# Kernel optimization log

Measured on AMD Instinct MI355X. Metric: run time of the kernel, lower is better.

The kernel has to match this reference:

```python
import jax, jax.numpy as jnp
import numpy as np

HEADS = 8

def _rotate_every_two(t):
    # t: [..., d]; interleaved rotation (-x2, x1) pairs
    x1 = t[..., ::2]
    x2 = t[..., 1::2]
    return jnp.stack([-x2, x1], axis=-1).reshape(t.shape)

def _theta_shift(t, sin, cos):
    return t * cos + _rotate_every_two(t) * sin

def setup_inputs() -> dict:
    key = jax.random.key(0)
    ks = jax.random.split(key, 5)
    B, H, W, C = 4, 40, 40, 512
    dh = C // HEADS
    x = jax.random.normal(ks[0], (B, H, W, C), dtype=jnp.float32)
    sin = jax.random.normal(ks[1], (H, W, dh), dtype=jnp.float32)
    cos = jax.random.normal(ks[2], (H, W, dh), dtype=jnp.float32)
    # 1x1 conv weight [3C, C] (kernel dims squeezed) + bias
    w_qkv = jax.random.normal(ks[3], (3 * C, C), dtype=jnp.float32) * (C ** -0.5)
    b_qkv = jnp.zeros((3 * C,), dtype=jnp.float32)
    return {"x": x, "sin": sin, "cos": cos, "w_qkv": w_qkv, "b_qkv": b_qkv}

def reference(x, sin, cos, w_qkv, b_qkv):
    B, H, W, C = x.shape
    heads = HEADS
    dh = C // heads
    scale = dh ** -0.5
    # 1x1 conv == per-pixel linear projection
    qkv = jnp.einsum('bhwc,oc->bhwo', x, w_qkv) + b_qkv  # [B,H,W,3C]
    q, k, v = jnp.split(qkv, 3, axis=-1)

    def to_heads(t):
        # channel order is (heads, dim_head) per the torch rearrange
        return t.reshape(B, H, W, heads, dh).transpose(0, 3, 1, 2, 4)  # [B,heads,H,W,dh]

    q = _theta_shift(to_heads(q), sin, cos)
    k = _theta_shift(to_heads(k), sin, cos)
    # v is computed but unused downstream in the original module (bug preserved)

    N = H * W
    q = q.reshape(B, heads, N, dh)
    k = k.reshape(B, heads, N, dh)

    attn = jnp.einsum('bhnd,bhmd->bhnm', q, k) * scale  # [B,heads,N,N]
    p = jax.nn.softmax(attn, axis=-1)
    # NOTE: original code does matmul(logist, kfine_heads) — K, not V. Kept faithful.
    out = jnp.einsum('bhnm,bhmd->bhnd', p, k)  # [B,heads,N,dh]
    out = out.transpose(0, 2, 1, 3).reshape(B, H, W, C)
    return out
```

## Files before the change

### kernel.cpp

```cpp
#include <hip/hip_runtime.h>
#include <hip/hip_bf16.h>


typedef __hip_bfloat16 bf16;
typedef __attribute__((ext_vector_type(8))) short short8;
typedef __attribute__((ext_vector_type(4))) short bfx4;
typedef __attribute__((ext_vector_type(4))) float f32x4;

#define NSP 1600
#define CDIM 512
#define DH 64

__device__ __forceinline__ f32x4 mfma32(short8 a, short8 b, f32x4 c) {
  return __builtin_amdgcn_mfma_f32_16x16x32_bf16(a, b, c, 0, 0, 0);
}

#if __has_builtin(__builtin_amdgcn_mfma_f32_16x16x16bf16_1k)
__device__ __forceinline__ f32x4 mfma_k16(bfx4 a, bfx4 b, f32x4 c) {
  return __builtin_amdgcn_mfma_f32_16x16x16bf16_1k(a, b, c, 0, 0, 0);
}
#else
__device__ __forceinline__ f32x4 mfma_k16(bfx4 a, bfx4 b, f32x4 c) {
  short8 a8 = {a.x, a.y, a.z, a.w, 0, 0, 0, 0};
  short8 b8 = {b.x, b.y, b.z, b.w, 0, 0, 0, 0};
  return __builtin_amdgcn_mfma_f32_16x16x32_bf16(a8, b8, c, 0, 0, 0);
}
#endif

__device__ __forceinline__ short8 cvt8(float4 v0, float4 v1) {
  short8 r; bf16* p = (bf16*)&r;
  p[0] = __float2bfloat16(v0.x); p[1] = __float2bfloat16(v0.y);
  p[2] = __float2bfloat16(v0.z); p[3] = __float2bfloat16(v0.w);
  p[4] = __float2bfloat16(v1.x); p[5] = __float2bfloat16(v1.y);
  p[6] = __float2bfloat16(v1.z); p[7] = __float2bfloat16(v1.w);
  return r;
}

extern "C" __global__ __launch_bounds__(256)
void cvt_kernel(const float* __restrict__ x, const float* __restrict__ w,
                const float* __restrict__ sin_t, const float* __restrict__ cos_t,
                bf16* __restrict__ x_bf, bf16* __restrict__ w_bf,
                float* __restrict__ sinT, float* __restrict__ cosT)
{
  __shared__ float t_lds[64][68];
  const int bid = blockIdx.x, tid = threadIdx.x;
  if (bid < 1600) {
    const size_t i = (size_t)bid * 2048 + tid * 8;
    float4 v0 = *(const float4*)(x + i);
    float4 v1 = *(const float4*)(x + i + 4);
    *(short8*)(x_bf + i) = cvt8(v0, v1);
  } else if (bid < 1856) {
    const size_t i = (size_t)(bid - 1600) * 2048 + tid * 8;
    float4 v0 = *(const float4*)(w + i);
    float4 v1 = *(const float4*)(w + i + 4);
    *(short8*)(w_bf + i) = cvt8(v0, v1);
  } else {
    const int t = bid - 1856;
    const float* src = (t < 25) ? sin_t : cos_t;
    float* dst = (t < 25) ? sinT : cosT;
    const int nt = (t < 25) ? t : t - 25;
    const int r = tid >> 2, c = (tid & 3) * 16;
#pragma unroll
    for (int j = 0; j < 4; ++j)
      *(float4*)&t_lds[r][c + j * 4] =
          *(const float4*)(src + (size_t)(nt * 64 + r) * 64 + c + j * 4);
    __syncthreads();
#pragma unroll
    for (int j4 = 0; j4 < 4; ++j4) {
      float4 o;
      o.x = t_lds[c + j4 * 4 + 0][r];
      o.y = t_lds[c + j4 * 4 + 1][r];
      o.z = t_lds[c + j4 * 4 + 2][r];
      o.w = t_lds[c + j4 * 4 + 3][r];
      *(float4*)(dst + (size_t)r * NSP + nt * 64 + c + j4 * 4) = o;
    }
  }
}

extern "C" __global__ __launch_bounds__(256)
void proj_kernel(const bf16* __restrict__ x_bf, const bf16* __restrict__ w_bf,
                 const float* __restrict__ bias, const float* __restrict__ sinT,
                 const float* __restrict__ cosT, bf16* __restrict__ q_ws,
                 bf16* __restrict__ k2_ws, bf16* __restrict__ kt2_ws)
{
  __shared__ __align__(16) char smem[36864];
  bf16 (*x_lds)[72] = (bf16(*)[72])smem;
  bf16 (*w_lds)[72] = (bf16(*)[72])(smem + 18432);
  bf16* ep = (bf16*)smem;

  const int tid  = threadIdx.x;
  const int wave = tid >> 6;
  const int lane = tid & 63;
  const int col  = lane & 15;
  const int quad = lane >> 4;
  const int wm = wave >> 1, wo = wave & 1;
  const int m0 = blockIdx.x * 128;
  const int o0 = blockIdx.y * 128;

  f32x4 acc[4][4];
#pragma unroll
  for (int i = 0; i < 4; ++i)
#pragma unroll
    for (int j = 0; j < 4; ++j) acc[i][j] = {0.f, 0.f, 0.f, 0.f};

  const int srow = tid >> 1;
  const int sch  = (tid & 1) * 32;

  for (int kt = 0; kt < 8; ++kt) {
    __syncthreads();
    {
      const bf16* xs = x_bf + (size_t)(m0 + srow) * CDIM + kt * 64 + sch;
      const bf16* ws = w_bf + (size_t)(o0 + srow) * CDIM + kt * 64 + sch;
#pragma unroll
      for (int j = 0; j < 4; ++j) {
        *(short8*)&x_lds[srow][sch + j * 8] = *(const short8*)(xs + j * 8);
        *(short8*)&w_lds[srow][sch + j * 8] = *(const short8*)(ws + j * 8);
      }
    }
    __syncthreads();
#pragma unroll
    for (int half = 0; half < 2; ++half) {
      short8 af[4], bfr[4];
#pragma unroll
      for (int mt = 0; mt < 4; ++mt)
        af[mt] = *(short8*)&x_lds[wm * 64 + mt * 16 + col][half * 32 + quad * 8];
#pragma unroll
      for (int ot = 0; ot < 4; ++ot)
        bfr[ot] = *(short8*)&w_lds[wo * 64 + ot * 16 + col][half * 32 + quad * 8];
#pragma unroll
      for (int mt = 0; mt < 4; ++mt)
#pragma unroll
        for (int ot = 0; ot < 4; ++ot)
          acc[mt][ot] = mfma32(af[mt], bfr[ot], acc[mt][ot]);
    }
  }

  __syncthreads();
  const int b_idx = (m0 + wm * 64) / NSP;
  const int n0w   = m0 + wm * 64 - b_idx * NSP;
  const bool isq  = (o0 < 512);
#pragma unroll
  for (int ot = 0; ot < 4; ++ot) {
    const int o_local = wo * 64 + ot * 16 + col;
    const int o_g = o0 + o_local;
    const float bv = bias[o_g];
    const int d = o_g & 63;
#pragma unroll
    for (int mt = 0; mt < 4; ++mt) {
      const int nl = mt * 16 + quad * 4;
      float t[4], rot[4];
#pragma unroll
      for (int r = 0; r < 4; ++r) t[r] = acc[mt][ot][r] + bv;
#pragma unroll
      for (int r = 0; r < 4; ++r) {
        float tp = __shfl_xor(t[r], 1, 64);
        rot[r] = (lane & 1) ? tp : -tp;
      }
      const float4 c4 = *(const float4*)(cosT + (size_t)d * NSP + n0w + nl);
      const float4 s4 = *(const float4*)(sinT + (size_t)d * NSP + n0w + nl);
      float res[4];
      res[0] = t[0] * c4.x + rot[0] * s4.x;
      res[1] = t[1] * c4.y + rot[1] * s4.y;
      res[2] = t[2] * c4.z + rot[2] * s4.z;
      res[3] = t[3] * c4.w + rot[3] * s4.w;
      if (isq) {
#pragma unroll
        for (int r = 0; r < 4; ++r) res[r] *= 0.125f;
      }
      bfx4 pk; bf16* pp = (bf16*)&pk;
#pragma unroll
      for (int r = 0; r < 4; ++r) pp[r] = __float2bfloat16(res[r]);
      *(bfx4*)&ep[o_local * 132 + wm * 64 + nl] = pk;
    }
  }
  __syncthreads();

  if (isq) {
    const int m_l = tid >> 1, half = tid & 1;
    const int gm = m0 + m_l;
    const int bi = gm / NSP, n = gm - bi * NSP;
    const int h = (o0 >> 6) + half;
    bf16* base = q_ws + ((size_t)(bi * 8 + h) * NSP + n) * 64;
#pragma unroll
    for (int c = 0; c < 8; ++c) {
      short8 v; bf16* vp = (bf16*)&v;
#pragma unroll
      for (int j = 0; j < 8; ++j) vp[j] = ep[(half * 64 + c * 8 + j) * 132 + m_l];
      *(short8*)(base + c * 8) = v;
    }
  } else {
    const int h0 = (o0 - 512) >> 6;
#pragma unroll
    for (int it = 0; it < 8; ++it) {
      const int ci = it * 256 + tid;
      const int hh = ci >> 10, T = (ci >> 9) & 1, inner = ci & 511;
      const int ccol = inner & 15, cq = (inner >> 4) & 3;
      const int f = (inner >> 6) & 1, ti = (inner >> 7) & 1, kh2 = (inner >> 8) & 1;
      const int gmb = m0 + T * 64;
      const int bi = gmb / NSP, ktile = (gmb - bi * NSP) >> 6;
      const int m_l = T * 64 + (2 * kh2 + ti) * 16 + ccol;
      const int er0 = hh * 64 + (f * 4 + cq) * 8;
      short8 v; bf16* vp = (bf16*)&v;
#pragma unroll
      for (int j = 0; j < 8; ++j) vp[j] = ep[(er0 + j) * 132 + m_l];
      *(short8*)(k2_ws +
          (((size_t)(bi * 8 + h0 + hh) * 25 + ktile) * 512 + inner) * 8) = v;
    }
#pragma unroll
    for (int it = 0; it < 8; ++it) {
      const int ci = it * 256 + tid;
      const int hh = ci >> 10, T = (ci >> 9) & 1, inner = ci & 511;
      const int ccol = inner & 15, cq = (inner >> 4) & 3;
      const int dt = (inner >> 6) & 3, kh2 = (inner >> 8) & 1;
      const int gmb = m0 + T * 64;
      const int bi = gmb / NSP, ktile = (gmb - bi * NSP) >> 6;
      const bf16* eprow =
          ep + (hh * 64 + dt * 16 + ccol) * 132 + T * 64 + kh2 * 32 + cq * 4;
      short8 v;
      ((bfx4*)&v)[0] = *(const bfx4*)(eprow);
      ((bfx4*)&v)[1] = *(const bfx4*)(eprow + 16);
      *(short8*)(kt2_ws +
          (((size_t)(bi * 8 + h0 + hh) * 25 + ktile) * 512 + inner) * 8) = v;
    }
  }
}

extern "C" __global__ __launch_bounds__(256)
void attn_kernel(const bf16* __restrict__ q_ws, const bf16* __restrict__ k2_ws,
                 const bf16* __restrict__ kt2_ws, float* __restrict__ out)
{
  __shared__ float red[2][64][36];

  const int qt = blockIdx.x, bh = blockIdx.y;
  const int b = bh >> 3, h = bh & 7;
  const int tid  = threadIdx.x;
  const int wave = tid >> 6;
  const int lane = tid & 63;
  const int col  = lane & 15;
  const int quad = lane >> 4;
  const int qg = wave & 1, kh = wave >> 1;

  short8 qb[2][2];
#pragma unroll
  for (int ct = 0; ct < 2; ++ct) {
    const bf16* qp =
        q_ws + ((size_t)bh * NSP + qt * 64 + (qg * 2 + ct) * 16 + col) * 64;
    qb[ct][0] = *(const short8*)(qp + quad * 8);
    qb[ct][1] = *(const short8*)(qp + 32 + quad * 8);
  }

  f32x4 oacc[4][2];
#pragma unroll
  for (int i = 0; i < 4; ++i)
#pragma unroll
    for (int j = 0; j < 2; ++j) oacc[i][j] = {0.f, 0.f, 0.f, 0.f};
  float l_part[2] = {0.f, 0.f};

  const bf16* k2b  = k2_ws  + (size_t)bh * 25 * 4096;
  const bf16* kt2b = kt2_ws + (size_t)bh * 25 * 4096;

  for (int kt = 0; kt < 25; ++kt) {
    const bf16* kc  = k2b  + kt * 4096;
    const bf16* kc2 = kt2b + kt * 4096;

    short8 kf[2][2];
#pragma unroll
    for (int ti = 0; ti < 2; ++ti)
#pragma unroll
      for (int f = 0; f < 2; ++f)
        kf[ti][f] =
            *(const short8*)(kc + (((kh * 2 + ti) * 2 + f) * 64 + lane) * 8);
    short8 ktf[4];
#pragma unroll
    for (int dt = 0; dt < 4; ++dt)
      ktf[dt] = *(const short8*)(kc2 + ((kh * 4 + dt) * 64 + lane) * 8);

    f32x4 s[2][2];
#pragma unroll
    for (int ti = 0; ti < 2; ++ti)
#pragma unroll
      for (int ct = 0; ct < 2; ++ct) {
        f32x4 t = {0.f, 0.f, 0.f, 0.f};
        t = mfma32(kf[ti][0], qb[ct][0], t);
        t = mfma32(kf[ti][1], qb[ct][1], t);
        s[ti][ct] = t;
      }

    bfx4 p4[2][2];
#pragma unroll
    for (int ti = 0; ti < 2; ++ti)
#pragma unroll
      for (int ct = 0; ct < 2; ++ct) {
#pragma unroll
        for (int r = 0; r < 4; ++r) s[ti][ct][r] = __expf(s[ti][ct][r]);
        l_part[ct] += s[ti][ct][0] + s[ti][ct][1] + s[ti][ct][2] + s[ti][ct][3];
        bf16* pp = (bf16*)&p4[ti][ct];
#pragma unroll
        for (int r = 0; r < 4; ++r) pp[r] = __float2bfloat16(s[ti][ct][r]);
      }

#pragma unroll
    for (int dt = 0; dt < 4; ++dt) {
      bfx4 alo = __builtin_shufflevector(ktf[dt], ktf[dt], 0, 1, 2, 3);
      bfx4 ahi = __builtin_shufflevector(ktf[dt], ktf[dt], 4, 5, 6, 7);
#pragma unroll
      for (int ct = 0; ct < 2; ++ct) {
        oacc[dt][ct] = mfma_k16(alo, p4[0][ct], oacc[dt][ct]);
        oacc[dt][ct] = mfma_k16(ahi, p4[1][ct], oacc[dt][ct]);
      }
    }
  }

#pragma unroll
  for (int ct = 0; ct < 2; ++ct) {
    l_part[ct] += __shfl_xor(l_part[ct], 16, 64);
    l_part[ct] += __shfl_xor(l_part[ct], 32, 64);
  }

  if (wave >= 2) {
    float* dst = &red[wave - 2][lane][0];
#pragma unroll
    for (int dt = 0; dt < 4; ++dt)
#pragma unroll
      for (int ct = 0; ct < 2; ++ct)
        *(f32x4*)(dst + (dt * 2 + ct) * 4) = oacc[dt][ct];
    dst[32] = l_part[0]; dst[33] = l_part[1];
  }
  __syncthreads();
  if (wave < 2) {
    const float* srcr = &red[wave][lane][0];
#pragma unroll
    for (int dt = 0; dt < 4; ++dt)
#pragma unroll
      for (int ct = 0; ct < 2; ++ct)
        oacc[dt][ct] += *(const f32x4*)(srcr + (dt * 2 + ct) * 4);
    const float inv0 = 1.f / (l_part[0] + srcr[32]);
    const float inv1 = 1.f / (l_part[1] + srcr[33]);
#pragma unroll
    for (int ct = 0; ct < 2; ++ct) {
      const float inv = ct ? inv1 : inv0;
      const int qrow = qt * 64 + (qg * 2 + ct) * 16 + col;
      float* ob = out + ((size_t)b * NSP + qrow) * CDIM + h * 64;
#pragma unroll
      for (int dt = 0; dt < 4; ++dt) {
        float4 v;
        v.x = oacc[dt][ct][0] * inv; v.y = oacc[dt][ct][1] * inv;
        v.z = oacc[dt][ct][2] * inv; v.w = oacc[dt][ct][3] * inv;
        *(float4*)(ob + dt * 16 + quad * 4) = v;
      }
    }
  }
}

extern "C" void kernel_launch(void* const* d_in, const int* in_sizes, int n_in,
                              void* d_out, int out_size, void* d_ws, size_t ws_size,
                              hipStream_t stream) {
  const float* x     = (const float*)d_in[0];
  const float* sin_t = (const float*)d_in[1];
  const float* cos_t = (const float*)d_in[2];
  const float* w_qkv = (const float*)d_in[3];
  const float* b_qkv = (const float*)d_in[4];
  float* out = (float*)d_out;

  const size_t QK = (size_t)32 * NSP * DH;
  bf16* q_ws   = (bf16*)d_ws;
  bf16* k2_ws  = q_ws + QK;
  bf16* kt2_ws = k2_ws + QK;
  bf16* x_bf   = kt2_ws + QK;
  bf16* w_bf   = x_bf + (size_t)6400 * CDIM;
  float* sinT  = (float*)(w_bf + (size_t)1024 * CDIM);
  float* cosT  = sinT + (size_t)DH * NSP;

  cvt_kernel<<<1906, 256, 0, stream>>>(x, w_qkv, sin_t, cos_t, x_bf, w_bf, sinT, cosT);

  dim3 gproj(50, 8);
  proj_kernel<<<gproj, 256, 0, stream>>>(x_bf, w_bf, b_qkv, sinT, cosT,
                                         q_ws, k2_ws, kt2_ws);

  dim3 gattn(25, 32);
  attn_kernel<<<gattn, 256, 0, stream>>>(q_ws, k2_ws, kt2_ws, out);
}
```

Before: 140.5 us.

## Split attention key tile across four waves and use exp2 with log2e-folded scale

Each wave now processes all 64 query rows against its own 16-key slice of each 64-key tile, instead of a 2x2 split of query groups and key halves. The K^T workspace layout is reordered to match this per-wave slicing. This loads each K fragment once per wave and reuses it across four query tiles, while the Q fragments and output accumulators grow. The q scaling now folds in log2(e) so the kernel can call exp2f instead of __expf. The final reduction is now a 4-way sum done by a single wave through a larger LDS buffer, which adds register pressure and a longer serial epilogue.

```diff
diff --git a/kernel.cpp b/kernel.cpp
--- a/kernel.cpp
+++ b/kernel.cpp
@@ -165,7 +165,7 @@
       res[3] = t[3] * c4.w + rot[3] * s4.w;
       if (isq) {
 #pragma unroll
-        for (int r = 0; r < 4; ++r) res[r] *= 0.125f;
+        for (int r = 0; r < 4; ++r) res[r] *= 0.1803368801111204f;
       }
       bfx4 pk; bf16* pp = (bf16*)&pk;
 #pragma unroll
@@ -211,14 +211,15 @@
       const int ci = it * 256 + tid;
       const int hh = ci >> 10, T = (ci >> 9) & 1, inner = ci & 511;
       const int ccol = inner & 15, cq = (inner >> 4) & 3;
-      const int dt = (inner >> 6) & 3, kh2 = (inner >> 8) & 1;
+      const int p = (inner >> 6) & 1, w2 = (inner >> 7) & 3;
       const int gmb = m0 + T * 64;
       const int bi = gmb / NSP, ktile = (gmb - bi * NSP) >> 6;
-      const bf16* eprow =
-          ep + (hh * 64 + dt * 16 + ccol) * 132 + T * 64 + kh2 * 32 + cq * 4;
+      const bf16* eplo =
+          ep + (hh * 64 + p * 32 + ccol) * 132 + T * 64 + w2 * 16 + cq * 4;
+      const bf16* ephi = eplo + 16 * 132;
       short8 v;
-      ((bfx4*)&v)[0] = *(const bfx4*)(eprow);
-      ((bfx4*)&v)[1] = *(const bfx4*)(eprow + 16);
+      ((bfx4*)&v)[0] = *(const bfx4*)eplo;
+      ((bfx4*)&v)[1] = *(const bfx4*)ephi;
       *(short8*)(kt2_ws +
           (((size_t)(bi * 8 + h0 + hh) * 25 + ktile) * 512 + inner) * 8) = v;
     }
@@ -229,7 +230,7 @@
 void attn_kernel(const bf16* __restrict__ q_ws, const bf16* __restrict__ k2_ws,
                  const bf16* __restrict__ kt2_ws, float* __restrict__ out)
 {
-  __shared__ float red[2][64][36];
+  __shared__ float red[3][64][68];
 
   const int qt = blockIdx.x, bh = blockIdx.y;
   const int b = bh >> 3, h = bh & 7;
@@ -238,23 +239,22 @@
   const int lane = tid & 63;
   const int col  = lane & 15;
   const int quad = lane >> 4;
-  const int qg = wave & 1, kh = wave >> 1;
-
-  short8 qb[2][2];
-#pragma unroll
-  for (int ct = 0; ct < 2; ++ct) {
+
+  short8 qb[4][2];
+#pragma unroll
+  for (int ct = 0; ct < 4; ++ct) {
     const bf16* qp =
-        q_ws + ((size_t)bh * NSP + qt * 64 + (qg * 2 + ct) * 16 + col) * 64;
+        q_ws + ((size_t)bh * NSP + qt * 64 + ct * 16 + col) * 64;
     qb[ct][0] = *(const short8*)(qp + quad * 8);
     qb[ct][1] = *(const short8*)(qp + 32 + quad * 8);
   }
 
-  f32x4 oacc[4][2];
+  f32x4 oacc[4][4];
 #pragma unroll
   for (int i = 0; i < 4; ++i)
 #pragma unroll
-    for (int j = 0; j < 2; ++j) oacc[i][j] = {0.f, 0.f, 0.f, 0.f};
-  float l_part[2] = {0.f, 0.f};
+    for (int j = 0; j < 4; ++j) oacc[i][j] = {0.f, 0.f, 0.f, 0.f};
+  float l_part[4] = {0.f, 0.f, 0.f, 0.f};
 
   const bf16* k2b  = k2_ws  + (size_t)bh * 25 * 4096;
   const bf16* kt2b = kt2_ws + (size_t)bh * 25 * 4096;
@@ -263,83 +263,77 @@
     const bf16* kc  = k2b  + kt * 4096;
     const bf16* kc2 = kt2b + kt * 4096;
 
-    short8 kf[2][2];
-#pragma unroll
-    for (int ti = 0; ti < 2; ++ti)
-#pragma unroll
-      for (int f = 0; f < 2; ++f)
-        kf[ti][f] =
-            *(const short8*)(kc + (((kh * 2 + ti) * 2 + f) * 64 + lane) * 8);
-    short8 ktf[4];
-#pragma unroll
-    for (int dt = 0; dt < 4; ++dt)
-      ktf[dt] = *(const short8*)(kc2 + ((kh * 4 + dt) * 64 + lane) * 8);
-
-    f32x4 s[2][2];
-#pragma unroll
-    for (int ti = 0; ti < 2; ++ti)
-#pragma unroll
-      for (int ct = 0; ct < 2; ++ct) {
-        f32x4 t = {0.f, 0.f, 0.f, 0.f};
-        t = mfma32(kf[ti][0], qb[ct][0], t);
-        t = mfma32(kf[ti][1], qb[ct][1], t);
-        s[ti][ct] = t;
-      }
-
-    bfx4 p4[2][2];
-#pragma unroll
-    for (int ti = 0; ti < 2; ++ti)
-#pragma unroll
-      for (int ct = 0; ct < 2; ++ct) {
-#pragma unroll
-        for (int r = 0; r < 4; ++r) s[ti][ct][r] = __expf(s[ti][ct][r]);
-        l_part[ct] += s[ti][ct][0] + s[ti][ct][1] + s[ti][ct][2] + s[ti][ct][3];
-        bf16* pp = (bf16*)&p4[ti][ct];
-#pragma unroll
-        for (int r = 0; r < 4; ++r) pp[r] = __float2bfloat16(s[ti][ct][r]);
-      }
-
-#pragma unroll
-    for (int dt = 0; dt < 4; ++dt) {
-      bfx4 alo = __builtin_shufflevector(ktf[dt], ktf[dt], 0, 1, 2, 3);
-      bfx4 ahi = __builtin_shufflevector(ktf[dt], ktf[dt], 4, 5, 6, 7);
-#pragma unroll
-      for (int ct = 0; ct < 2; ++ct) {
-        oacc[dt][ct] = mfma_k16(alo, p4[0][ct], oacc[dt][ct]);
-        oacc[dt][ct] = mfma_k16(ahi, p4[1][ct], oacc[dt][ct]);
-      }
-    }
-  }
-
-#pragma unroll
-  for (int ct = 0; ct < 2; ++ct) {
+    short8 kf0 = *(const short8*)(kc  + ((wave * 2 + 0) * 64 + lane) * 8);
+    short8 kf1 = *(const short8*)(kc  + ((wave * 2 + 1) * 64 + lane) * 8);
+    short8 kt0 = *(const short8*)(kc2 + ((wave * 2 + 0) * 64 + lane) * 8);
+    short8 kt1 = *(const short8*)(kc2 + ((wave * 2 + 1) * 64 + lane) * 8);
+
+    f32x4 s[4];
+#pragma unroll
+    for (int ct = 0; ct < 4; ++ct) {
+      f32x4 t = {0.f, 0.f, 0.f, 0.f};
+      t = mfma32(kf0, qb[ct][0], t);
+      t = mfma32(kf1, qb[ct][1], t);
+      s[ct] = t;
+    }
+
+    bfx4 p4[4];
+#pragma unroll
+    for (int ct = 0; ct < 4; ++ct) {
+#pragma unroll
+      for (int r = 0; r < 4; ++r) s[ct][r] = exp2f(s[ct][r]);
+      l_part[ct] += s[ct][0] + s[ct][1] + s[ct][2] + s[ct][3];
+      bf16* pp = (bf16*)&p4[ct];
+#pragma unroll
+      for (int r = 0; r < 4; ++r) pp[r] = __float2bfloat16(s[ct][r]);
+    }
+
+    bfx4 a0 = __builtin_shufflevector(kt0, kt0, 0, 1, 2, 3);
+    bfx4 a1 = __builtin_shufflevector(kt0, kt0, 4, 5, 6, 7);
+    bfx4 a2 = __builtin_shufflevector(kt1, kt1, 0, 1, 2, 3);
+    bfx4 a3 = __builtin_shufflevector(kt1, kt1, 4, 5, 6, 7);
+#pragma unroll
+    for (int ct = 0; ct < 4; ++ct) {
+      oacc[0][ct] = mfma_k16(a0, p4[ct], oacc[0][ct]);
+      oacc[1][ct] = mfma_k16(a1, p4[ct], oacc[1][ct]);
+      oacc[2][ct] = mfma_k16(a2, p4[ct], oacc[2][ct]);
+      oacc[3][ct] = mfma_k16(a3, p4[ct], oacc[3][ct]);
+    }
+  }
+
+#pragma unroll
+  for (int ct = 0; ct < 4; ++ct) {
     l_part[ct] += __shfl_xor(l_part[ct], 16, 64);
     l_part[ct] += __shfl_xor(l_part[ct], 32, 64);
   }
 
-  if (wave >= 2) {
-    float* dst = &red[wave - 2][lane][0];
+  if (wave >= 1) {
+    float* dst = &red[wave - 1][lane][0];
 #pragma unroll
     for (int dt = 0; dt < 4; ++dt)
 #pragma unroll
-      for (int ct = 0; ct < 2; ++ct)
-        *(f32x4*)(dst + (dt * 2 + ct) * 4) = oacc[dt][ct];
-    dst[32] = l_part[0]; dst[33] = l_part[1];
+      for (int ct = 0; ct < 4; ++ct)
+        *(f32x4*)(dst + (dt * 4 + ct) * 4) = oacc[dt][ct];
+#pragma unroll
+    for (int ct = 0; ct < 4; ++ct) dst[64 + ct] = l_part[ct];
   }
   __syncthreads();
-  if (wave < 2) {
-    const float* srcr = &red[wave][lane][0];
-#pragma unroll
-    for (int dt = 0; dt < 4; ++dt)
-#pragma unroll
-      for (int ct = 0; ct < 2; ++ct)
-        oacc[dt][ct] += *(const f32x4*)(srcr + (dt * 2 + ct) * 4);
-    const float inv0 = 1.f / (l_part[0] + srcr[32]);
-    const float inv1 = 1.f / (l_part[1] + srcr[33]);
-#pragma unroll
-    for (int ct = 0; ct < 2; ++ct) {
-      const float inv = ct ? inv1 : inv0;
-      const int qrow = qt * 64 + (qg * 2 + ct) * 16 + col;
+  if (wave == 0) {
+#pragma unroll
+    for (int wsrc = 0; wsrc < 3; ++wsrc) {
+      const float* srcr = &red[wsrc][lane][0];
+#pragma unroll
+      for (int dt = 0; dt < 4; ++dt)
+#pragma unroll
+        for (int ct = 0; ct < 4; ++ct)
+          oacc[dt][ct] += *(const f32x4*)(srcr + (dt * 4 + ct) * 4);
+#pragma unroll
+      for (int ct = 0; ct < 4; ++ct) l_part[ct] += srcr[64 + ct];
+    }
+#pragma unroll
+    for (int ct = 0; ct < 4; ++ct) {
+      const float inv = 1.f / l_part[ct];
+      const int qrow = qt * 64 + ct * 16 + col;
       float* ob = out + ((size_t)b * NSP + qrow) * CDIM + h * 64;
 #pragma unroll
       for (int dt = 0; dt < 4; ++dt) {
```

New measurement: 156.3 us. 11.2% more time.

## Halve attention query tile per block and fold log2e into Q scale for exp2

Applied to the files above, without the earlier changes.

Each attention block now handles 32 query rows instead of 64, so the grid doubles to 50x32 blocks and each wave keeps a single 16-column query tile. This gives more blocks to fill the CUs and cuts register pressure, but every block now rereads the full K stream for half as many queries. The Q prescale now includes log2(e), so the softmax can use exp2f in place of __expf. Without max subtraction, overflow behaviour stays the same as before.

```diff
diff --git a/kernel.cpp b/kernel.cpp
--- a/kernel.cpp
+++ b/kernel.cpp
@@ -165,7 +165,7 @@
       res[3] = t[3] * c4.w + rot[3] * s4.w;
       if (isq) {
 #pragma unroll
-        for (int r = 0; r < 4; ++r) res[r] *= 0.125f;
+        for (int r = 0; r < 4; ++r) res[r] *= 0.1803368801111204f;
       }
       bfx4 pk; bf16* pp = (bf16*)&pk;
 #pragma unroll
@@ -229,7 +229,7 @@
 void attn_kernel(const bf16* __restrict__ q_ws, const bf16* __restrict__ k2_ws,
                  const bf16* __restrict__ kt2_ws, float* __restrict__ out)
 {
-  __shared__ float red[2][64][36];
+  __shared__ float red[2][64][20];
 
   const int qt = blockIdx.x, bh = blockIdx.y;
   const int b = bh >> 3, h = bh & 7;
@@ -240,21 +240,18 @@
   const int quad = lane >> 4;
   const int qg = wave & 1, kh = wave >> 1;
 
-  short8 qb[2][2];
-#pragma unroll
-  for (int ct = 0; ct < 2; ++ct) {
+  short8 qb0, qb1;
+  {
     const bf16* qp =
-        q_ws + ((size_t)bh * NSP + qt * 64 + (qg * 2 + ct) * 16 + col) * 64;
-    qb[ct][0] = *(const short8*)(qp + quad * 8);
-    qb[ct][1] = *(const short8*)(qp + 32 + quad * 8);
-  }
-
-  f32x4 oacc[4][2];
-#pragma unroll
-  for (int i = 0; i < 4; ++i)
-#pragma unroll
-    for (int j = 0; j < 2; ++j) oacc[i][j] = {0.f, 0.f, 0.f, 0.f};
-  float l_part[2] = {0.f, 0.f};
+        q_ws + ((size_t)bh * NSP + qt * 32 + qg * 16 + col) * 64;
+    qb0 = *(const short8*)(qp + quad * 8);
+    qb1 = *(const short8*)(qp + 32 + quad * 8);
+  }
+
+  f32x4 oacc[4];
+#pragma unroll
+  for (int i = 0; i < 4; ++i) oacc[i] = {0.f, 0.f, 0.f, 0.f};
+  float l_part = 0.f;
 
   const bf16* k2b  = k2_ws  + (size_t)bh * 25 * 4096;
   const bf16* kt2b = kt2_ws + (size_t)bh * 25 * 4096;
@@ -263,91 +260,79 @@
     const bf16* kc  = k2b  + kt * 4096;
     const bf16* kc2 = kt2b + kt * 4096;
 
-    short8 kf[2][2];
-#pragma unroll
-    for (int ti = 0; ti < 2; ++ti)
-#pragma unroll
-      for (int f = 0; f < 2; ++f)
-        kf[ti][f] =
-            *(const short8*)(kc + (((kh * 2 + ti) * 2 + f) * 64 + lane) * 8);
-    short8 ktf[4];
-#pragma unroll
-    for (int dt = 0; dt < 4; ++dt)
-      ktf[dt] = *(const short8*)(kc2 + ((kh * 4 + dt) * 64 + lane) * 8);
-
-    f32x4 s[2][2];
-#pragma unroll
-    for (int ti = 0; ti < 2; ++ti)
-#pragma unroll
-      for (int ct = 0; ct < 2; ++ct) {
-        f32x4 t = {0.f, 0.f, 0.f, 0.f};
-        t = mfma32(kf[ti][0], qb[ct][0], t);
-        t = mfma32(kf[ti][1], qb[ct][1], t);
-        s[ti][ct] = t;
-      }
-
-    bfx4 p4[2][2];
-#pragma unroll
-    for (int ti = 0; ti < 2; ++ti)
-#pragma unroll
-      for (int ct = 0; ct < 2; ++ct) {
-#pragma unroll
-        for (int r = 0; r < 4; ++r) s[ti][ct][r] = __expf(s[ti][ct][r]);
-        l_part[ct] += s[ti][ct][0] + s[ti][ct][1] + s[ti][ct][2] + s[ti][ct][3];
-        bf16* pp = (bf16*)&p4[ti][ct];
-#pragma unroll
-        for (int r = 0; r < 4; ++r) pp[r] = __float2bfloat16(s[ti][ct][r]);
-      }
-
-#pragma unroll
-    for (int dt = 0; dt < 4; ++dt) {
-      bfx4 alo = __builtin_shufflevector(ktf[dt], ktf[dt], 0, 1, 2, 3);
-      bfx4 ahi = __builtin_shufflevector(ktf[dt], ktf[dt], 4, 5, 6, 7);
-#pragma unroll
-      for (int ct = 0; ct < 2; ++ct) {
-        oacc[dt][ct] = mfma_k16(alo, p4[0][ct], oacc[dt][ct]);
-        oacc[dt][ct] = mfma_k16(ahi, p4[1][ct], oacc[dt][ct]);
-      }
-    }
-  }
-
-#pragma unroll
-  for (int ct = 0; ct < 2; ++ct) {
-    l_part[ct] += __shfl_xor(l_part[ct], 16, 64);
-    l_part[ct] += __shfl_xor(l_part[ct], 32, 64);
-  }
+    short8 kf00 = *(const short8*)(kc + (((kh * 2 + 0) * 2 + 0) * 64 + lane) * 8);
+    short8 kf01 = *(const short8*)(kc + (((kh * 2 + 0) * 2 + 1) * 64 + lane) * 8);
+    short8 kf10 = *(const short8*)(kc + (((kh * 2 + 1) * 2 + 0) * 64 + lane) * 8);
+    short8 kf11 = *(const short8*)(kc + (((kh * 2 + 1) * 2 + 1) * 64 + lane) * 8);
+    short8 ktf0 = *(const short8*)(kc2 + ((kh * 4 + 0) * 64 + lane) * 8);
+    short8 ktf1 = *(const short8*)(kc2 + ((kh * 4 + 1) * 64 + lane) * 8);
+    short8 ktf2 = *(const short8*)(kc2 + ((kh * 4 + 2) * 64 + lane) * 8);
+    short8 ktf3 = *(const short8*)(kc2 + ((kh * 4 + 3) * 64 + lane) * 8);
+
+    f32x4 s0 = {0.f, 0.f, 0.f, 0.f}, s1 = {0.f, 0.f, 0.f, 0.f};
+    s0 = mfma32(kf00, qb0, s0); s0 = mfma32(kf01, qb1, s0);
+    s1 = mfma32(kf10, qb0, s1); s1 = mfma32(kf11, qb1, s1);
+
+    bfx4 p0, p1;
+    {
+      bf16* pp0 = (bf16*)&p0; bf16* pp1 = (bf16*)&p1;
+#pragma unroll
+      for (int r = 0; r < 4; ++r) {
+        s0[r] = exp2f(s0[r]); s1[r] = exp2f(s1[r]);
+      }
+      l_part += s0[0] + s0[1] + s0[2] + s0[3] + s1[0] + s1[1] + s1[2] + s1[3];
+#pragma unroll
+      for (int r = 0; r < 4; ++r) {
+        pp0[r] = __float2bfloat16(s0[r]);
+        pp1[r] = __float2bfloat16(s1[r]);
+      }
+    }
+
+    {
+      bfx4 a0 = __builtin_shufflevector(ktf0, ktf0, 0, 1, 2, 3);
+      bfx4 a0h = __builtin_shufflevector(ktf0, ktf0, 4, 5, 6, 7);
+      bfx4 a1 = __builtin_shufflevector(ktf1, ktf1, 0, 1, 2, 3);
+      bfx4 a1h = __builtin_shufflevector(ktf1, ktf1, 4, 5, 6, 7);
+      bfx4 a2 = __builtin_shufflevector(ktf2, ktf2, 0, 1, 2, 3);
+      bfx4 a2h = __builtin_shufflevector(ktf2, ktf2, 4, 5, 6, 7);
+      bfx4 a3 = __builtin_shufflevector(ktf3, ktf3, 0, 1, 2, 3);
+      bfx4 a3h = __builtin_shufflevector(ktf3, ktf3, 4, 5, 6, 7);
+      oacc[0] = mfma_k16(a0,  p0, oacc[0]);
+      oacc[0] = mfma_k16(a0h, p1, oacc[0]);
+      oacc[1] = mfma_k16(a1,  p0, oacc[1]);
+      oacc[1] = mfma_k16(a1h, p1, oacc[1]);
+      oacc[2] = mfma_k16(a2,  p0, oacc[2]);
+      oacc[2] = mfma_k16(a2h, p1, oacc[2]);
+      oacc[3] = mfma_k16(a3,  p0, oacc[3]);
+      oacc[3] = mfma_k16(a3h, p1, oacc[3]);
+    }
+  }
+
+  l_part += __shfl_xor(l_part, 16, 64);
+  l_part += __shfl_xor(l_part, 32, 64);
 
   if (wave >= 2) {
     float* dst = &red[wave - 2][lane][0];
 #pragma unroll
     for (int dt = 0; dt < 4; ++dt)
-#pragma unroll
-      for (int ct = 0; ct < 2; ++ct)
-        *(f32x4*)(dst + (dt * 2 + ct) * 4) = oacc[dt][ct];
-    dst[32] = l_part[0]; dst[33] = l_part[1];
+      *(f32x4*)(dst + dt * 4) = oacc[dt];
+    dst[16] = l_part;
   }
   __syncthreads();
   if (wave < 2) {
     const float* srcr = &red[wave][lane][0];
 #pragma unroll
     for (int dt = 0; dt < 4; ++dt)
-#pragma unroll
-      for (int ct = 0; ct < 2; ++ct)
-        oacc[dt][ct] += *(const f32x4*)(srcr + (dt * 2 + ct) * 4);
-    const float inv0 = 1.f / (l_part[0] + srcr[32]);
-    const float inv1 = 1.f / (l_part[1] + srcr[33]);
-#pragma unroll
-    for (int ct = 0; ct < 2; ++ct) {
-      const float inv = ct ? inv1 : inv0;
-      const int qrow = qt * 64 + (qg * 2 + ct) * 16 + col;
-      float* ob = out + ((size_t)b * NSP + qrow) * CDIM + h * 64;
-#pragma unroll
-      for (int dt = 0; dt < 4; ++dt) {
-        float4 v;
-        v.x = oacc[dt][ct][0] * inv; v.y = oacc[dt][ct][1] * inv;
-        v.z = oacc[dt][ct][2] * inv; v.w = oacc[dt][ct][3] * inv;
-        *(float4*)(ob + dt * 16 + quad * 4) = v;
-      }
+      oacc[dt] += *(const f32x4*)(srcr + dt * 4);
+    const float inv = 1.f / (l_part + srcr[16]);
+    const int qrow = qt * 32 + qg * 16 + col;
+    float* ob = out + ((size_t)b * NSP + qrow) * CDIM + h * 64;
+#pragma unroll
+    for (int dt = 0; dt < 4; ++dt) {
+      float4 v;
+      v.x = oacc[dt][0] * inv; v.y = oacc[dt][1] * inv;
+      v.z = oacc[dt][2] * inv; v.w = oacc[dt][3] * inv;
+      *(float4*)(ob + dt * 16 + quad * 4) = v;
     }
   }
 }
@@ -377,6 +362,6 @@
   proj_kernel<<<gproj, 256, 0, stream>>>(x_bf, w_bf, b_qkv, sinT, cosT,
                                          q_ws, k2_ws, kt2_ws);
 
-  dim3 gattn(25, 32);
+  dim3 gattn(50, 32);
   attn_kernel<<<gattn, 256, 0, stream>>>(q_ws, k2_ws, kt2_ws, out);
 }
```

New measurement: 148.5 us. 1.06x slower.
